# Optimization experiments

Hardware: AMD Instinct MI355X
Metric: run time of the kernel (lower is better)

The kernel has to match this reference:

```python
import jax, jax.numpy as jnp
import numpy as np

H = 256  # rnn hidden size

def _rnn_dir(x, wih, whh, bih, bhh):
    # x: [B,T,D] -> outputs [B,T,H]; h_t = tanh(x_t Wih^T + bih + h_{t-1} Whh^T + bhh)
    xproj = jnp.einsum('btd,hd->bth', x, wih) + bih + bhh  # precompute input projection
    def step(h, xp):
        h = jnp.tanh(xp + h @ whh.T)
        return h, h
    h0 = jnp.zeros((x.shape[0], whh.shape[0]), x.dtype)
    _, ys = jax.lax.scan(step, h0, jnp.swapaxes(xproj, 0, 1))
    return jnp.swapaxes(ys, 0, 1)

def _birnn(x, wif, whf, bif, bhf, wib, whb, bib, bhb):
    fwd = _rnn_dir(x, wif, whf, bif, bhf)
    bwd = _rnn_dir(x[:, ::-1, :], wib, whb, bib, bhb)[:, ::-1, :]
    return jnp.concatenate([fwd, bwd], axis=-1)

def setup_inputs() -> dict:
    key = jax.random.key(0)
    ks = jax.random.split(key, 24)
    B, T, V, E = 64, 512, 131072, 128
    s = 0.05
    emb = jax.random.normal(ks[0], (V, E), jnp.float32) * s
    emb = emb.at[0].set(0.0)  # padding_idx=0
    def W(k, shp):
        return jax.random.normal(k, shp, jnp.float32) * s
    inp = {
        'x': jax.random.randint(ks[1], (B, T), 0, V),
        'emb': emb,
        'r1_wif': W(ks[2], (H, E)), 'r1_whf': W(ks[3], (H, H)),
        'r1_bif': W(ks[4], (H,)), 'r1_bhf': W(ks[5], (H,)),
        'r1_wib': W(ks[6], (H, E)), 'r1_whb': W(ks[7], (H, H)),
        'r1_bib': W(ks[8], (H,)), 'r1_bhb': W(ks[9], (H,)),
        'r2_wif': W(ks[10], (H, 2 * H)), 'r2_whf': W(ks[11], (H, H)),
        'r2_bif': W(ks[12], (H,)), 'r2_bhf': W(ks[13], (H,)),
        'r2_wib': W(ks[14], (H, 2 * H)), 'r2_whb': W(ks[15], (H, H)),
        'r2_bib': W(ks[16], (H,)), 'r2_bhb': W(ks[17], (H,)),
        'ln_g': jnp.ones((1024,), jnp.float32),
        'ln_b': jnp.zeros((1024,), jnp.float32),
        'w1': W(ks[18], (512, 1024)), 'b1': W(ks[19], (512,)),
        'w2': W(ks[20], (256, 512)), 'b2': W(ks[21], (256,)),
    }
    return inp

def reference(x, emb, r1_wif, r1_whf, r1_bif, r1_bhf, r1_wib, r1_whb, r1_bib, r1_bhb,
              r2_wif, r2_whf, r2_bif, r2_bhf, r2_wib, r2_whb, r2_bib, r2_bhb,
              ln_g, ln_b, w1, b1, w2, b2):
    e = emb[x]  # [B,T,128]
    o1 = _birnn(e, r1_wif, r1_whf, r1_bif, r1_bhf, r1_wib, r1_whb, r1_bib, r1_bhb)  # [B,T,512]
    o2 = _birnn(o1, r2_wif, r2_whf, r2_bif, r2_bhf, r2_wib, r2_whb, r2_bib, r2_bhb)  # [B,T,512]
    last = o2[:, -1, :]
    mean = jnp.mean(o2, axis=1)
    h = jnp.concatenate([last, mean], axis=1)  # [B,1024]
    mu = jnp.mean(h, axis=-1, keepdims=True)
    var = jnp.mean(jnp.square(h - mu), axis=-1, keepdims=True)
    h = (h - mu) * jax.lax.rsqrt(var + 1e-5) * ln_g + ln_b
    h = jax.nn.relu(h @ w1.T + b1)
    return h @ w2.T + b2
```

## Files before the change

### kernel.cpp

```cpp
#include <hip/hip_runtime.h>
#include <stdint.h>

typedef unsigned short u16;
typedef unsigned int   u32;
typedef __attribute__((ext_vector_type(8))) short short8;
typedef __attribute__((ext_vector_type(4))) float f32x4;

#define T_LEN 512
#define HID   256
#define C2LE 2.8853900817779268f

__device__ __forceinline__ float bflo(u32 u){ union{u32 i; float f;} v; v.i = u << 16; return v.f; }
__device__ __forceinline__ float bfhi(u32 u){ union{u32 i; float f;} v; v.i = u & 0xffff0000u; return v.f; }
__device__ __forceinline__ float b2f(u16 s){ union{u32 i; float f;} v; v.i = ((u32)s) << 16; return v.f; }
__device__ __forceinline__ u16 f2b(float f){
  union{float f; u32 i;} v; v.f = f;
  u32 r = v.i + 0x7fffu + ((v.i >> 16) & 1u);
  return (u16)(r >> 16);
}
__device__ __forceinline__ u32 pk2(float a, float b){ return (u32)f2b(a) | ((u32)f2b(b) << 16); }
__device__ __forceinline__ u32 cvtpk(float a, float b){
  u32 r; asm("v_cvt_pk_bf16_f32 %0, %1, %2" : "=v"(r) : "v"(a), "v"(b)); return r;
}
__device__ __forceinline__ float tanh_pre(float y){
#if __has_builtin(__builtin_amdgcn_exp2f)
  float e = __builtin_amdgcn_exp2f(y);
#else
  float e = exp2f(y);
#endif
  return __builtin_fmaf(-2.f, __builtin_amdgcn_rcpf(e + 1.f), 1.f);
}
__device__ __forceinline__ bool flag_bf16(const u32* f){ return (f[0] & 0xFFFFu) == 0x3F80u; }

#define NT 22
struct ConvArgs {
  const void* src[NT];
  u32 off[NT];
  u32 total;
  const u32* flagsrc;
};

__global__ __launch_bounds__(256)
void convert_params(ConvArgs a, u16* __restrict__ dst)
{
  const bool bf = flag_bf16(a.flagsrc);
  const u32 stride = gridDim.x * blockDim.x;
  for (u32 g = blockIdx.x * blockDim.x + threadIdx.x; g < a.total; g += stride) {
    int t = 0;
    #pragma unroll
    for (int i = 1; i < NT; ++i) t += (g >= a.off[i]);
    u32 local = g - a.off[t];
    float v = bf ? b2f(((const u16*)a.src[t])[local])
                 : ((const float*)a.src[t])[local];
    if (t == 1 || t == 5 || t == 9 || t == 13) v *= C2LE;
    dst[g] = f2b(v);
  }
}

template<int K, int SRC>
__global__ __launch_bounds__(256, 2)
void wgemm(const void* Bsrc, const int* __restrict__ gidx,
           const u16* __restrict__ Wf, const u16* __restrict__ Wb,
           const u16* __restrict__ bif, const u16* __restrict__ bhf,
           const u16* __restrict__ bib, const u16* __restrict__ bhb,
           u16* outT, const u32* flagsrc)
{
  __shared__ __align__(16) u16 lds[64 * K];
  const int tid  = threadIdx.x;
  const int row0 = blockIdx.x * 64;
  const int bb   = row0 >> 9;
  const int t0   = row0 & 511;
  const int bt   = bb >> 4, nb = bb & 15;
  constexpr int CPR = K / 8;

  bool abf = true;
  if (SRC == 0) abf = flag_bf16(flagsrc);

  for (int i = tid; i < 64 * CPR; i += 256) {
    int r = i / CPR, c = i % CPR;
    uint4 v;
    if (SRC == 0) {
      long rb = (long)gidx[row0 + r] * K;
      if (abf) {
        v = *(const uint4*)((const u16*)Bsrc + rb + c * 8);
      } else {
        const float* af = (const float*)Bsrc;
        float4 lo = *(const float4*)(af + rb + c * 8);
        float4 hi = *(const float4*)(af + rb + c * 8 + 4);
        v.x = pk2(lo.x, lo.y); v.y = pk2(lo.z, lo.w);
        v.z = pk2(hi.x, hi.y); v.w = pk2(hi.z, hi.w);
      }
    } else {
      int k = c * 8, d = k >> 8;
      size_t e = (size_t)(d * 4 + bt) * 2097152 + (size_t)(t0 + r) * 4096
               + (size_t)nb * 256 + (k & 255);
      v = *(const uint4*)((const u16*)Bsrc + e);
    }
    *(uint4*)&lds[r * K + ((c ^ (r & 7)) * 8)] = v;
  }
  __syncthreads();

  const int w = tid >> 6, lane = tid & 63, n16 = lane & 15, quad = lane >> 4;
  const int d = w >> 1;
  const u16* W  = d ? Wb : Wf;
  const u16* bi = d ? bib : bif;
  const u16* bh = d ? bhb : bhf;
  const int mbase = (w & 1) * 128;

  f32x4 acc[8][4];
  #pragma unroll
  for (int i = 0; i < 8; ++i)
    #pragma unroll
    for (int j = 0; j < 4; ++j) acc[i][j] = (f32x4){0.f, 0.f, 0.f, 0.f};

  #pragma unroll
  for (int kk = 0; kk < K / 32; ++kk) {
    short8 bfr[4];
    #pragma unroll
    for (int j = 0; j < 4; ++j) {
      int r = j * 16 + n16;
      int c = (kk * 4 + quad) ^ (r & 7);
      bfr[j] = *(const short8*)&lds[r * K + c * 8];
    }
    #pragma unroll
    for (int i = 0; i < 8; ++i) {
      short8 afr = *(const short8*)(W + (size_t)(mbase + i * 16 + n16) * K + kk * 32 + quad * 8);
      #pragma unroll
      for (int j = 0; j < 4; ++j)
        acc[i][j] = __builtin_amdgcn_mfma_f32_16x16x32_bf16(afr, bfr[j], acc[i][j], 0, 0, 0);
    }
  }

  #pragma unroll
  for (int i = 0; i < 8; ++i) {
    int mrow0 = mbase + i * 16 + quad * 4;
    uint2 biv = *(const uint2*)(bi + mrow0);
    uint2 bhv = *(const uint2*)(bh + mrow0);
    float bias0 = b2f(biv.x & 0xffff) + b2f(bhv.x & 0xffff);
    float bias1 = b2f(biv.x >> 16)    + b2f(bhv.x >> 16);
    float bias2 = b2f(biv.y & 0xffff) + b2f(bhv.y & 0xffff);
    float bias3 = b2f(biv.y >> 16)    + b2f(bhv.y >> 16);
    #pragma unroll
    for (int j = 0; j < 4; ++j) {
      int t = t0 + j * 16 + n16;
      uint2 pv;
      pv.x = cvtpk(C2LE * (acc[i][j][0] + bias0), C2LE * (acc[i][j][1] + bias1));
      pv.y = cvtpk(C2LE * (acc[i][j][2] + bias2), C2LE * (acc[i][j][3] + bias3));
      size_t e = (size_t)(d * 4 + bt) * 2097152 + (size_t)t * 4096
               + (size_t)nb * 256 + mrow0;
      *(uint2*)(outT + e) = pv;
    }
  }
}

template<int MODE>
__device__ __forceinline__ void scan_step5(
    int s, int send,
    const u16* hrp, u16* hwp, uint2& pf,
    const u16*& xptr, u16*& optr, int pstep,
    const short8 (&wa)[8], f32x4& sum, float* lastb, int lbase)
{
  short8 hb[8];
  #pragma unroll
  for (int kk = 0; kk < 8; ++kk)
    hb[kk] = *(const short8*)(hrp + kk * 32);

  uint2 xv = pf;
  pf = *(const uint2*)(xptr);
  xptr += pstep;

  f32x4 a = (f32x4){bflo(xv.x), bfhi(xv.x), bflo(xv.y), bfhi(xv.y)};
  f32x4 b = (f32x4){0.f, 0.f, 0.f, 0.f};
  #pragma unroll
  for (int kk = 0; kk < 8; kk += 2) {
    a = __builtin_amdgcn_mfma_f32_16x16x32_bf16(wa[kk],     hb[kk],     a, 0, 0, 0);
    b = __builtin_amdgcn_mfma_f32_16x16x32_bf16(wa[kk + 1], hb[kk + 1], b, 0, 0, 0);
  }

  float h0 = tanh_pre(a[0] + b[0]);
  float h1 = tanh_pre(a[1] + b[1]);
  float h2 = tanh_pre(a[2] + b[2]);
  float h3 = tanh_pre(a[3] + b[3]);
  uint2 hv; hv.x = cvtpk(h0, h1); hv.y = cvtpk(h2, h3);
  *(uint2*)(hwp) = hv;

  if (MODE == 0) {
    *(uint2*)(optr) = hv;
    optr += pstep;
  } else {
    sum += (f32x4){h0, h1, h2, h3};
    if (s == send)
      *(float4*)&lastb[lbase] = (float4){h0, h1, h2, h3};
  }

  asm volatile("s_waitcnt lgkmcnt(0)" ::: "memory");
  __builtin_amdgcn_s_barrier();
  asm volatile("" ::: "memory");
}

template<int MODE>
__global__ __launch_bounds__(1024, 4)
void rnn_scan(const u16* xpT,
              const u16* __restrict__ whhF, const u16* __restrict__ whhB,
              u16* o1T, float* __restrict__ lastb, float* __restrict__ sumb)
{
  __shared__ __align__(16) u16 hl[2][16][264];
  const int tid = threadIdx.x, w = tid >> 6, lane = tid & 63;
  const int n16 = lane & 15, quad = lane >> 4;
  const int dir = blockIdx.x >> 2, bt = blockIdx.x & 3;
  const u16* whh = dir ? whhB : whhF;
  const int m0 = w * 16 + quad * 4;

  short8 wa[8];
  #pragma unroll
  for (int kk = 0; kk < 8; ++kk)
    wa[kk] = *(const short8*)(whh + (size_t)(w * 16 + n16) * 256 + kk * 32 + quad * 8);

  for (int i = tid; i < 16 * 264; i += 1024) ((u16*)hl[0])[i] = 0;

  const size_t blkbase = (size_t)(dir * 4 + bt) * 2097152;
  const int t0    = dir ? 511 : 0;
  const int pstep = dir ? -4096 : 4096;
  const u16* xptr = xpT + blkbase + (size_t)t0 * 4096 + n16 * 256 + m0;
  u16*       optr = o1T + blkbase + (size_t)t0 * 4096 + n16 * 256 + m0;
  const int lbase = (dir * 64 + bt * 16 + n16) * 256 + m0;
  const int send  = dir ? 0 : 511;

  const u16* hr0 = &hl[0][n16][quad * 8];
  const u16* hr1 = &hl[1][n16][quad * 8];
  u16* hw0 = &hl[1][n16][m0];
  u16* hw1 = &hl[0][n16][m0];

  uint2 pf0, pf1;
  pf0 = *(const uint2*)(xptr); xptr += pstep;
  pf1 = *(const uint2*)(xptr); xptr += pstep;

  f32x4 sum = (f32x4){0.f, 0.f, 0.f, 0.f};
  __syncthreads();

  for (int s = 0; s < 512; s += 2) {
    scan_step5<MODE>(s,     send, hr0, hw0, pf0, xptr, optr, pstep, wa, sum, lastb, lbase);
    scan_step5<MODE>(s + 1, send, hr1, hw1, pf1, xptr, optr, pstep, wa, sum, lastb, lbase);
  }

  if (MODE == 1)
    *(float4*)&sumb[lbase] = (float4){sum[0], sum[1], sum[2], sum[3]};
}

__device__ __forceinline__ void scan_step8(
    int s, int send,
    const u16* hrp, u16* hwp, uint2 (&pf)[2],
    const u16*& xptr, int pstep,
    const short8 (&wa)[2][8], f32x4 (&sum)[2], float* lastb, int lbase)
{
  short8 hb[8];
  #pragma unroll
  for (int kk = 0; kk < 8; ++kk)
    hb[kk] = *(const short8*)(hrp + kk * 32);

  uint2 xv0 = pf[0], xv1 = pf[1];
  pf[0] = *(const uint2*)(xptr);
  pf[1] = *(const uint2*)(xptr + 16);
  xptr += pstep;

  f32x4 a0 = (f32x4){bflo(xv0.x), bfhi(xv0.x), bflo(xv0.y), bfhi(xv0.y)};
  f32x4 a1 = (f32x4){bflo(xv1.x), bfhi(xv1.x), bflo(xv1.y), bfhi(xv1.y)};
  f32x4 b0 = (f32x4){0.f, 0.f, 0.f, 0.f};
  f32x4 b1 = (f32x4){0.f, 0.f, 0.f, 0.f};
  #pragma unroll
  for (int kk = 0; kk < 8; kk += 2) {
    a0 = __builtin_amdgcn_mfma_f32_16x16x32_bf16(wa[0][kk],     hb[kk],     a0, 0, 0, 0);
    a1 = __builtin_amdgcn_mfma_f32_16x16x32_bf16(wa[1][kk],     hb[kk],     a1, 0, 0, 0);
    b0 = __builtin_amdgcn_mfma_f32_16x16x32_bf16(wa[0][kk + 1], hb[kk + 1], b0, 0, 0, 0);
    b1 = __builtin_amdgcn_mfma_f32_16x16x32_bf16(wa[1][kk + 1], hb[kk + 1], b1, 0, 0, 0);
  }

  float h00 = tanh_pre(a0[0] + b0[0]), h01 = tanh_pre(a0[1] + b0[1]);
  float h02 = tanh_pre(a0[2] + b0[2]), h03 = tanh_pre(a0[3] + b0[3]);
  float h10 = tanh_pre(a1[0] + b1[0]), h11 = tanh_pre(a1[1] + b1[1]);
  float h12 = tanh_pre(a1[2] + b1[2]), h13 = tanh_pre(a1[3] + b1[3]);

  uint2 hv0; hv0.x = cvtpk(h00, h01); hv0.y = cvtpk(h02, h03);
  uint2 hv1; hv1.x = cvtpk(h10, h11); hv1.y = cvtpk(h12, h13);
  *(uint2*)(hwp)      = hv0;
  *(uint2*)(hwp + 16) = hv1;

  sum[0] += (f32x4){h00, h01, h02, h03};
  sum[1] += (f32x4){h10, h11, h12, h13};
  if (s == send) {
    *(float4*)&lastb[lbase]      = (float4){h00, h01, h02, h03};
    *(float4*)&lastb[lbase + 16] = (float4){h10, h11, h12, h13};
  }

  asm volatile("s_waitcnt lgkmcnt(0)" ::: "memory");
  __builtin_amdgcn_s_barrier();
  asm volatile("" ::: "memory");
}

__global__ __launch_bounds__(512, 2)
void rnn_scan8(const u16* xpT,
               const u16* __restrict__ whhF, const u16* __restrict__ whhB,
               float* __restrict__ lastb, float* __restrict__ sumb)
{
  __shared__ __align__(16) u16 hl[2][16][264];
  const int tid = threadIdx.x, w = tid >> 6, lane = tid & 63;
  const int n16 = lane & 15, quad = lane >> 4;
  const int dir = blockIdx.x >> 2, bt = blockIdx.x & 3;
  const u16* whh = dir ? whhB : whhF;

  short8 wa[2][8];
  #pragma unroll
  for (int j = 0; j < 2; ++j)
    #pragma unroll
    for (int kk = 0; kk < 8; ++kk)
      wa[j][kk] = *(const short8*)(whh + (size_t)(w * 32 + j * 16 + n16) * 256
                                       + kk * 32 + quad * 8);

  for (int i = tid; i < 16 * 264; i += 512) ((u16*)hl[0])[i] = 0;

  const size_t blkbase = (size_t)(dir * 4 + bt) * 2097152;
  const int t0    = dir ? 511 : 0;
  const int pstep = dir ? -4096 : 4096;
  const int m0    = w * 32 + quad * 4;
  const u16* xptr = xpT + blkbase + (size_t)t0 * 4096 + n16 * 256 + m0;
  const int lbase = (dir * 64 + bt * 16 + n16) * 256 + m0;
  const int send  = dir ? 0 : 511;

  const u16* hr0 = &hl[0][n16][quad * 8];
  const u16* hr1 = &hl[1][n16][quad * 8];
  u16* hw0 = &hl[1][n16][m0];
  u16* hw1 = &hl[0][n16][m0];

  uint2 pf0[2], pf1[2];
  pf0[0] = *(const uint2*)(xptr);
  pf0[1] = *(const uint2*)(xptr + 16);
  xptr += pstep;
  pf1[0] = *(const uint2*)(xptr);
  pf1[1] = *(const uint2*)(xptr + 16);
  xptr += pstep;

  f32x4 sum[2];
  sum[0] = (f32x4){0.f, 0.f, 0.f, 0.f};
  sum[1] = (f32x4){0.f, 0.f, 0.f, 0.f};
  __syncthreads();

  for (int s = 0; s < 512; s += 2) {
    scan_step8(s,     send, hr0, hw0, pf0, xptr, pstep, wa, sum, lastb, lbase);
    scan_step8(s + 1, send, hr1, hw1, pf1, xptr, pstep, wa, sum, lastb, lbase);
  }

  *(float4*)&sumb[lbase]      = (float4){sum[0][0], sum[0][1], sum[0][2], sum[0][3]};
  *(float4*)&sumb[lbase + 16] = (float4){sum[1][0], sum[1][1], sum[1][2], sum[1][3]};
}

__device__ __forceinline__ float dot8(uint4 q, const float* hp){
  return bflo(q.x)*hp[0] + bfhi(q.x)*hp[1] + bflo(q.y)*hp[2] + bfhi(q.y)*hp[3]
       + bflo(q.z)*hp[4] + bfhi(q.z)*hp[5] + bflo(q.w)*hp[6] + bfhi(q.w)*hp[7];
}

__global__ __launch_bounds__(256)
void head_kernel(const float* __restrict__ lastb, const float* __restrict__ sumb,
                 const u16* __restrict__ g, const u16* __restrict__ be,
                 const u16* __restrict__ w1, const u16* __restrict__ b1,
                 const u16* __restrict__ w2, const u16* __restrict__ b2,
                 void* outv, const u32* flagsrc)
{
  __shared__ __align__(16) float hv[1024];
  __shared__ __align__(16) float act[512];
  __shared__ float red[8];
  const int tid = threadIdx.x;
  const int b   = blockIdx.x;
  const bool bf = flag_bf16(flagsrc);

  float v0 = lastb[b * 256 + tid];
  float v1 = lastb[(64 + b) * 256 + tid];
  float v2 = sumb[b * 256 + tid] * (1.f / 512.f);
  float v3 = sumb[(64 + b) * 256 + tid] * (1.f / 512.f);
  hv[tid] = v0; hv[256 + tid] = v1; hv[512 + tid] = v2; hv[768 + tid] = v3;

  float s  = v0 + v1 + v2 + v3;
  float ss = v0*v0 + v1*v1 + v2*v2 + v3*v3;
  #pragma unroll
  for (int off = 32; off; off >>= 1) {
    s  += __shfl_down(s, off);
    ss += __shfl_down(ss, off);
  }
  if ((tid & 63) == 0) { red[tid >> 6] = s; red[4 + (tid >> 6)] = ss; }
  __syncthreads();
  float S  = red[0] + red[1] + red[2] + red[3];
  float SS = red[4] + red[5] + red[6] + red[7];
  float mu   = S * (1.f / 1024.f);
  float var  = SS * (1.f / 1024.f) - mu * mu;
  float rstd = rsqrtf(var + 1e-5f);

  #pragma unroll
  for (int i = 0; i < 4; ++i) {
    int idx = i * 256 + tid;
    hv[idx] = (hv[idx] - mu) * rstd * b2f(g[idx]) + b2f(be[idx]);
  }
  __syncthreads();

  #pragma unroll
  for (int jj = 0; jj < 2; ++jj) {
    int j = jj * 256 + tid;
    const uint4* wr = (const uint4*)(w1 + (long)j * 1024);
    float a = 0.f;
    for (int c = 0; c < 128; ++c) a += dot8(wr[c], &hv[c * 8]);
    a += b2f(b1[j]);
    act[j] = a > 0.f ? a : 0.f;
  }
  __syncthreads();

  const uint4* wr2 = (const uint4*)(w2 + (long)tid * 512);
  float a = 0.f;
  for (int c = 0; c < 64; ++c) a += dot8(wr2[c], &act[c * 8]);
  a += b2f(b2[tid]);

  if (bf) {
    ((u16*)outv)[b * 256 + tid] = f2b(a);
  } else {
    union { u32 i; float f; } u; u.i = ((u32)f2b(a)) << 16;
    ((float*)outv)[b * 256 + tid] = u.f;
  }
}

extern "C" void kernel_launch(void* const* d_in, const int* in_sizes, int n_in,
                              void* d_out, int out_size, void* d_ws, size_t ws_size,
                              hipStream_t stream)
{
  const int* x    = (const int*)d_in[0];
  const u32* flag = (const u32*)d_in[18];

  static const int sizes[NT] = {
    32768, 65536, 256, 256, 32768, 65536, 256, 256,
    131072, 65536, 256, 256, 131072, 65536, 256, 256,
    1024, 1024, 524288, 512, 131072, 256
  };
  ConvArgs ca;
  u32 off = 0;
  for (int i = 0; i < NT; ++i) {
    ca.src[i] = d_in[2 + i];
    ca.off[i] = off;
    off += (u32)sizes[i];
  }
  ca.total = off;
  ca.flagsrc = flag;

  char* ws = (char*)d_ws;
  u16*   buf    = (u16*)ws;
  u16*   pm     = (u16*)(ws + 33554432);
  float* lastb  = (float*)(ws + 36054528);
  float* sumb   = (float*)(ws + 36185600);

  const u16* p_r1wif = pm + 0;
  const u16* p_r1whf = pm + 32768;
  const u16* p_r1bif = pm + 98304;
  const u16* p_r1bhf = pm + 98560;
  const u16* p_r1wib = pm + 98816;
  const u16* p_r1whb = pm + 131584;
  const u16* p_r1bib = pm + 197120;
  const u16* p_r1bhb = pm + 197376;
  const u16* p_r2wif = pm + 197632;
  const u16* p_r2whf = pm + 328704;
  const u16* p_r2bif = pm + 394240;
  const u16* p_r2bhf = pm + 394496;
  const u16* p_r2wib = pm + 394752;
  const u16* p_r2whb = pm + 525824;
  const u16* p_r2bib = pm + 591360;
  const u16* p_r2bhb = pm + 591616;
  const u16* p_lng   = pm + 591872;
  const u16* p_lnb   = pm + 592896;
  const u16* p_w1    = pm + 593920;
  const u16* p_b1    = pm + 1118208;
  const u16* p_w2    = pm + 1118720;
  const u16* p_b2    = pm + 1249792;

  convert_params<<<1024, 256, 0, stream>>>(ca, pm);

  wgemm<128, 0><<<512, 256, 0, stream>>>(d_in[1], x,
      p_r1wif, p_r1wib, p_r1bif, p_r1bhf, p_r1bib, p_r1bhb, buf, flag);
  rnn_scan<0><<<8, 1024, 0, stream>>>(buf, p_r1whf, p_r1whb, buf, nullptr, nullptr);
  wgemm<512, 1><<<512, 256, 0, stream>>>(buf, nullptr,
      p_r2wif, p_r2wib, p_r2bif, p_r2bhf, p_r2bib, p_r2bhb, buf, flag);
  rnn_scan8<<<8, 512, 0, stream>>>(buf, p_r2whf, p_r2whb, lastb, sumb);
  head_kernel<<<64, 256, 0, stream>>>(lastb, sumb, p_lng, p_lnb, p_w1, p_b1, p_w2, p_b2,
      d_out, flag);
}
```

Before: 929.8 us.

## Split RNN scan batch tiles across twice as many workgroups

Both recurrent scan kernels now cover 8 batch rows per workgroup instead of 16 and launch 16 workgroups instead of 8. Each workgroup still runs the full 16-column MFMA, but lanes for the duplicated rows skip their stores. The intent is to spread the serial 512-step recurrence over more CUs, so each step has less LDS traffic and barrier work per CU, at the cost of half-wasted MFMA work. The second-layer scan also raises wave priority around the MFMA block with s_setprio and interleaves the tanh, store and sum work for the two output tiles.

```diff
diff --git a/kernel.cpp b/kernel.cpp
--- a/kernel.cpp
+++ b/kernel.cpp
@@ -154,8 +154,8 @@
 }
 
 template<int MODE>
-__device__ __forceinline__ void scan_step5(
-    int s, int send,
+__device__ __forceinline__ void scan_step6(
+    int s, int send, bool st,
     const u16* hrp, u16* hwp, uint2& pf,
     const u16*& xptr, u16*& optr, int pstep,
     const short8 (&wa)[8], f32x4& sum, float* lastb, int lbase)
@@ -182,14 +182,14 @@
   float h2 = tanh_pre(a[2] + b[2]);
   float h3 = tanh_pre(a[3] + b[3]);
   uint2 hv; hv.x = cvtpk(h0, h1); hv.y = cvtpk(h2, h3);
-  *(uint2*)(hwp) = hv;
+  if (st) *(uint2*)(hwp) = hv;
 
   if (MODE == 0) {
-    *(uint2*)(optr) = hv;
+    if (st) *(uint2*)(optr) = hv;
     optr += pstep;
   } else {
     sum += (f32x4){h0, h1, h2, h3};
-    if (s == send)
+    if (s == send && st)
       *(float4*)&lastb[lbase] = (float4){h0, h1, h2, h3};
   }
 
@@ -198,38 +198,45 @@
   asm volatile("" ::: "memory");
 }
 
-template<int MODE>
+template<int MODE, int NB>
 __global__ __launch_bounds__(1024, 4)
 void rnn_scan(const u16* xpT,
               const u16* __restrict__ whhF, const u16* __restrict__ whhB,
               u16* o1T, float* __restrict__ lastb, float* __restrict__ sumb)
 {
-  __shared__ __align__(16) u16 hl[2][16][264];
+  __shared__ __align__(16) u16 hl[2][NB][264];
   const int tid = threadIdx.x, w = tid >> 6, lane = tid & 63;
   const int n16 = lane & 15, quad = lane >> 4;
-  const int dir = blockIdx.x >> 2, bt = blockIdx.x & 3;
-  const u16* whh = dir ? whhB : whhF;
-  const int m0 = w * 16 + quad * 4;
+  constexpr int NSUB = 16 / NB;
+  constexpr int NBLK = 4 * NSUB;
+  const int dir   = blockIdx.x / NBLK;
+  const int rbl   = blockIdx.x % NBLK;
+  const int bt    = rbl / NSUB;
+  const int nbase = (rbl % NSUB) * NB;
+  const int rb    = n16 & (NB - 1);
+  const bool st   = (n16 < NB);
+  const u16* whh  = dir ? whhB : whhF;
+  const int m0    = w * 16 + quad * 4;
 
   short8 wa[8];
   #pragma unroll
   for (int kk = 0; kk < 8; ++kk)
     wa[kk] = *(const short8*)(whh + (size_t)(w * 16 + n16) * 256 + kk * 32 + quad * 8);
 
-  for (int i = tid; i < 16 * 264; i += 1024) ((u16*)hl[0])[i] = 0;
+  for (int i = tid; i < NB * 264; i += 1024) ((u16*)hl[0])[i] = 0;
 
   const size_t blkbase = (size_t)(dir * 4 + bt) * 2097152;
   const int t0    = dir ? 511 : 0;
   const int pstep = dir ? -4096 : 4096;
-  const u16* xptr = xpT + blkbase + (size_t)t0 * 4096 + n16 * 256 + m0;
-  u16*       optr = o1T + blkbase + (size_t)t0 * 4096 + n16 * 256 + m0;
-  const int lbase = (dir * 64 + bt * 16 + n16) * 256 + m0;
+  const u16* xptr = xpT + blkbase + (size_t)t0 * 4096 + (size_t)(nbase + rb) * 256 + m0;
+  u16*       optr = o1T + blkbase + (size_t)t0 * 4096 + (size_t)(nbase + rb) * 256 + m0;
+  const int lbase = (dir * 64 + bt * 16 + nbase + rb) * 256 + m0;
   const int send  = dir ? 0 : 511;
 
-  const u16* hr0 = &hl[0][n16][quad * 8];
-  const u16* hr1 = &hl[1][n16][quad * 8];
-  u16* hw0 = &hl[1][n16][m0];
-  u16* hw1 = &hl[0][n16][m0];
+  const u16* hr0 = &hl[0][rb][quad * 8];
+  const u16* hr1 = &hl[1][rb][quad * 8];
+  u16* hw0 = &hl[1][rb][m0];
+  u16* hw1 = &hl[0][rb][m0];
 
   uint2 pf0, pf1;
   pf0 = *(const uint2*)(xptr); xptr += pstep;
@@ -239,16 +246,16 @@
   __syncthreads();
 
   for (int s = 0; s < 512; s += 2) {
-    scan_step5<MODE>(s,     send, hr0, hw0, pf0, xptr, optr, pstep, wa, sum, lastb, lbase);
-    scan_step5<MODE>(s + 1, send, hr1, hw1, pf1, xptr, optr, pstep, wa, sum, lastb, lbase);
-  }
-
-  if (MODE == 1)
+    scan_step6<MODE>(s,     send, st, hr0, hw0, pf0, xptr, optr, pstep, wa, sum, lastb, lbase);
+    scan_step6<MODE>(s + 1, send, st, hr1, hw1, pf1, xptr, optr, pstep, wa, sum, lastb, lbase);
+  }
+
+  if (MODE == 1 && st)
     *(float4*)&sumb[lbase] = (float4){sum[0], sum[1], sum[2], sum[3]};
 }
 
-__device__ __forceinline__ void scan_step8(
-    int s, int send,
+__device__ __forceinline__ void scan_step9(
+    int s, int send, bool st,
     const u16* hrp, u16* hwp, uint2 (&pf)[2],
     const u16*& xptr, int pstep,
     const short8 (&wa)[2][8], f32x4 (&sum)[2], float* lastb, int lbase)
@@ -263,6 +270,7 @@
   pf[1] = *(const uint2*)(xptr + 16);
   xptr += pstep;
 
+  __builtin_amdgcn_s_setprio(1);
   f32x4 a0 = (f32x4){bflo(xv0.x), bfhi(xv0.x), bflo(xv0.y), bfhi(xv0.y)};
   f32x4 a1 = (f32x4){bflo(xv1.x), bfhi(xv1.x), bflo(xv1.y), bfhi(xv1.y)};
   f32x4 b0 = (f32x4){0.f, 0.f, 0.f, 0.f};
@@ -274,20 +282,21 @@
     b0 = __builtin_amdgcn_mfma_f32_16x16x32_bf16(wa[0][kk + 1], hb[kk + 1], b0, 0, 0, 0);
     b1 = __builtin_amdgcn_mfma_f32_16x16x32_bf16(wa[1][kk + 1], hb[kk + 1], b1, 0, 0, 0);
   }
+  __builtin_amdgcn_s_setprio(0);
 
   float h00 = tanh_pre(a0[0] + b0[0]), h01 = tanh_pre(a0[1] + b0[1]);
   float h02 = tanh_pre(a0[2] + b0[2]), h03 = tanh_pre(a0[3] + b0[3]);
+  uint2 hv0; hv0.x = cvtpk(h00, h01); hv0.y = cvtpk(h02, h03);
+  if (st) *(uint2*)(hwp) = hv0;
+  sum[0] += (f32x4){h00, h01, h02, h03};
+
   float h10 = tanh_pre(a1[0] + b1[0]), h11 = tanh_pre(a1[1] + b1[1]);
   float h12 = tanh_pre(a1[2] + b1[2]), h13 = tanh_pre(a1[3] + b1[3]);
-
-  uint2 hv0; hv0.x = cvtpk(h00, h01); hv0.y = cvtpk(h02, h03);
   uint2 hv1; hv1.x = cvtpk(h10, h11); hv1.y = cvtpk(h12, h13);
-  *(uint2*)(hwp)      = hv0;
-  *(uint2*)(hwp + 16) = hv1;
-
-  sum[0] += (f32x4){h00, h01, h02, h03};
+  if (st) *(uint2*)(hwp + 16) = hv1;
   sum[1] += (f32x4){h10, h11, h12, h13};
-  if (s == send) {
+
+  if (s == send && st) {
     *(float4*)&lastb[lbase]      = (float4){h00, h01, h02, h03};
     *(float4*)&lastb[lbase + 16] = (float4){h10, h11, h12, h13};
   }
@@ -298,15 +307,21 @@
 }
 
 __global__ __launch_bounds__(512, 2)
-void rnn_scan8(const u16* xpT,
+void rnn_scan9(const u16* xpT,
                const u16* __restrict__ whhF, const u16* __restrict__ whhB,
                float* __restrict__ lastb, float* __restrict__ sumb)
 {
-  __shared__ __align__(16) u16 hl[2][16][264];
+  __shared__ __align__(16) u16 hl[2][8][264];
   const int tid = threadIdx.x, w = tid >> 6, lane = tid & 63;
   const int n16 = lane & 15, quad = lane >> 4;
-  const int dir = blockIdx.x >> 2, bt = blockIdx.x & 3;
-  const u16* whh = dir ? whhB : whhF;
+  const int dir   = blockIdx.x >> 3;
+  const int rbl   = blockIdx.x & 7;
+  const int bt    = rbl >> 1;
+  const int nbase = (rbl & 1) * 8;
+  const int rb    = n16 & 7;
+  const bool st   = (n16 < 8);
+  const u16* whh  = dir ? whhB : whhF;
+  const int m0    = w * 32 + quad * 4;
 
   short8 wa[2][8];
   #pragma unroll
@@ -316,20 +331,19 @@
       wa[j][kk] = *(const short8*)(whh + (size_t)(w * 32 + j * 16 + n16) * 256
                                        + kk * 32 + quad * 8);
 
-  for (int i = tid; i < 16 * 264; i += 512) ((u16*)hl[0])[i] = 0;
+  for (int i = tid; i < 8 * 264; i += 512) ((u16*)hl[0])[i] = 0;
 
   const size_t blkbase = (size_t)(dir * 4 + bt) * 2097152;
   const int t0    = dir ? 511 : 0;
   const int pstep = dir ? -4096 : 4096;
-  const int m0    = w * 32 + quad * 4;
-  const u16* xptr = xpT + blkbase + (size_t)t0 * 4096 + n16 * 256 + m0;
-  const int lbase = (dir * 64 + bt * 16 + n16) * 256 + m0;
+  const u16* xptr = xpT + blkbase + (size_t)t0 * 4096 + (size_t)(nbase + rb) * 256 + m0;
+  const int lbase = (dir * 64 + bt * 16 + nbase + rb) * 256 + m0;
   const int send  = dir ? 0 : 511;
 
-  const u16* hr0 = &hl[0][n16][quad * 8];
-  const u16* hr1 = &hl[1][n16][quad * 8];
-  u16* hw0 = &hl[1][n16][m0];
-  u16* hw1 = &hl[0][n16][m0];
+  const u16* hr0 = &hl[0][rb][quad * 8];
+  const u16* hr1 = &hl[1][rb][quad * 8];
+  u16* hw0 = &hl[1][rb][m0];
+  u16* hw1 = &hl[0][rb][m0];
 
   uint2 pf0[2], pf1[2];
   pf0[0] = *(const uint2*)(xptr);
@@ -345,12 +359,14 @@
   __syncthreads();
 
   for (int s = 0; s < 512; s += 2) {
-    scan_step8(s,     send, hr0, hw0, pf0, xptr, pstep, wa, sum, lastb, lbase);
-    scan_step8(s + 1, send, hr1, hw1, pf1, xptr, pstep, wa, sum, lastb, lbase);
-  }
-
-  *(float4*)&sumb[lbase]      = (float4){sum[0][0], sum[0][1], sum[0][2], sum[0][3]};
-  *(float4*)&sumb[lbase + 16] = (float4){sum[1][0], sum[1][1], sum[1][2], sum[1][3]};
+    scan_step9(s,     send, st, hr0, hw0, pf0, xptr, pstep, wa, sum, lastb, lbase);
+    scan_step9(s + 1, send, st, hr1, hw1, pf1, xptr, pstep, wa, sum, lastb, lbase);
+  }
+
+  if (st) {
+    *(float4*)&sumb[lbase]      = (float4){sum[0][0], sum[0][1], sum[0][2], sum[0][3]};
+    *(float4*)&sumb[lbase + 16] = (float4){sum[1][0], sum[1][1], sum[1][2], sum[1][3]};
+  }
 }
 
 __device__ __forceinline__ float dot8(uint4 q, const float* hp){
@@ -479,10 +495,10 @@
 
   wgemm<128, 0><<<512, 256, 0, stream>>>(d_in[1], x,
       p_r1wif, p_r1wib, p_r1bif, p_r1bhf, p_r1bib, p_r1bhb, buf, flag);
-  rnn_scan<0><<<8, 1024, 0, stream>>>(buf, p_r1whf, p_r1whb, buf, nullptr, nullptr);
+  rnn_scan<0, 8><<<16, 1024, 0, stream>>>(buf, p_r1whf, p_r1whb, buf, nullptr, nullptr);
   wgemm<512, 1><<<512, 256, 0, stream>>>(buf, nullptr,
       p_r2wif, p_r2wib, p_r2bif, p_r2bhf, p_r2bib, p_r2bhb, buf, flag);
-  rnn_scan8<<<8, 512, 0, stream>>>(buf, p_r2whf, p_r2whb, lastb, sumb);
+  rnn_scan9<<<16, 512, 0, stream>>>(buf, p_r2whf, p_r2whb, lastb, sumb);
   head_kernel<<<64, 256, 0, stream>>>(lastb, sumb, p_lng, p_lnb, p_w1, p_b1, p_w2, p_b2,
       d_out, flag);
 }
```

Result: faster. 886.1 us (-4.7%).
